# Kernel tuning notes

Measured on AMD Instinct MI355X. Metric: run time of the kernel, lower is better.

Reference implementation:

```python
import jax, jax.numpy as jnp
import numpy as np

NUM_CONN = 8

def _ein_reduce(f):
    # Einstein t-norm fold over last axis: T(a,b) = ab / (2 - (a+b-ab))
    acc = f[..., 0]
    for i in range(1, f.shape[-1]):
        b = f[..., i]
        ab = acc * b
        acc = ab / (2.0 - (acc + b - ab))
    return acc

def _coein_reduce(f):
    # Einstein t-conorm fold over last axis: S(a,b) = (a+b) / (1 + ab)
    acc = f[..., 0]
    for i in range(1, f.shape[-1]):
        b = f[..., i]
        acc = (acc + b) / (1.0 + acc * b)
    return acc

def _ddlg_layer(x, w, idx, is_train):
    # x: [B, in], idx: [out, C] int, w: [out, 4]
    feats = x[:, idx]                      # [B, out, C] gather
    ops = jnp.stack([
        jnp.min(feats, axis=-1),
        jnp.max(feats, axis=-1),
        _ein_reduce(feats),
        _coein_reduce(feats),
    ], axis=-1)                            # [B, out, 4]
    if is_train:
        prob = jax.nn.softmax(w, axis=-1)  # [out, 4]
    else:
        prob = jax.nn.one_hot(jnp.argmax(w, axis=-1), 4, dtype=x.dtype)
    return jnp.einsum('bof,of->bo', ops, prob)

def setup_inputs() -> dict:
    key = jax.random.key(0)
    ks = jax.random.split(key, 6)
    sizes = [4096, 2048, 1024, 2048, 4096]
    x = jax.random.uniform(ks[0], (4096, sizes[0]), dtype=jnp.float32)
    ws = [jax.random.normal(ks[1 + i], (sizes[i + 1], 4), dtype=jnp.float32) for i in range(4)]
    rng = np.random.default_rng(0)
    idxs = []
    for i in range(4):
        # randperm-without-replacement per output neuron
        perm = np.argsort(rng.random((sizes[i + 1], sizes[i])), axis=-1)[:, :NUM_CONN]
        idxs.append(jnp.asarray(perm, dtype=jnp.int32))
    return {
        'x': x,
        'w0': ws[0], 'w1': ws[1], 'w2': ws[2], 'w3': ws[3],
        'idx0': idxs[0], 'idx1': idxs[1], 'idx2': idxs[2], 'idx3': idxs[3],
        'is_train': 1,
    }

def reference(x, w0, w1, w2, w3, idx0, idx1, idx2, idx3, is_train):
    h = _ddlg_layer(x, w0, idx0, is_train)
    h = _ddlg_layer(h, w1, idx1, is_train)
    h = _ddlg_layer(h, w2, idx2, is_train)
    h = _ddlg_layer(h, w3, idx3, is_train)
    return h
```

## Files before the change

kernel.cpp:

```cpp
#include <hip/hip_runtime.h>


typedef _Float16 h2 __attribute__((ext_vector_type(2)));
typedef _Float16 h4 __attribute__((ext_vector_type(4)));

__device__ __forceinline__ float fastrcp(float x) { return __builtin_amdgcn_rcpf(x); }
__device__ __forceinline__ _Float16 hrcp(_Float16 x) {
#if __has_builtin(__builtin_amdgcn_rcph)
    return __builtin_amdgcn_rcph(x);
#else
    return (_Float16)__builtin_amdgcn_rcpf((float)x);
#endif
}
__device__ __forceinline__ unsigned packh2(float a, float b) {
    h2 v = {(_Float16)a, (_Float16)b};
    return __builtin_bit_cast(unsigned, v);
}
__device__ __forceinline__ h2 ash2(unsigned u) { return __builtin_bit_cast(h2, u); }

__device__ __forceinline__ unsigned pk_min(unsigned a, unsigned b) {
    unsigned d; asm("v_pk_min_f16 %0, %1, %2" : "=v"(d) : "v"(a), "v"(b)); return d;
}
__device__ __forceinline__ unsigned pk_max(unsigned a, unsigned b) {
    unsigned d; asm("v_pk_max_f16 %0, %1, %2" : "=v"(d) : "v"(a), "v"(b)); return d;
}
__device__ __forceinline__ unsigned pk_mul(unsigned a, unsigned b) {
    unsigned d; asm("v_pk_mul_f16 %0, %1, %2" : "=v"(d) : "v"(a), "v"(b)); return d;
}
__device__ __forceinline__ unsigned pk_add(unsigned a, unsigned b) {
    unsigned d; asm("v_pk_add_f16 %0, %1, %2" : "=v"(d) : "v"(a), "v"(b)); return d;
}
__device__ __forceinline__ unsigned pk_sub(unsigned a, unsigned b) {
    unsigned d;
    asm("v_pk_add_f16 %0, %1, %2 neg_lo:[0,1] neg_hi:[0,1]" : "=v"(d) : "v"(a), "v"(b));
    return d;
}
__device__ __forceinline__ unsigned pk_fma(unsigned a, unsigned b, unsigned c) {
    unsigned d;
    asm("v_pk_fma_f16 %0, %1, %2, %3" : "=v"(d) : "v"(a), "v"(b), "v"(c));
    return d;
}
__device__ __forceinline__ unsigned pk_fnma(unsigned a, unsigned b, unsigned c) {
    unsigned d;
    asm("v_pk_fma_f16 %0, %1, %2, %3 neg_lo:[1,0,0] neg_hi:[1,0,0]"
        : "=v"(d) : "v"(a), "v"(b), "v"(c));
    return d;
}
__device__ __forceinline__ unsigned pk_mul_blo(unsigned a, unsigned b) {
    unsigned d;
    asm("v_pk_mul_f16 %0, %1, %2 op_sel:[0,0] op_sel_hi:[1,0]" : "=v"(d) : "v"(a), "v"(b));
    return d;
}
__device__ __forceinline__ unsigned pk_fma_bhi(unsigned a, unsigned b, unsigned c) {
    unsigned d;
    asm("v_pk_fma_f16 %0, %1, %2, %3 op_sel:[0,1,0] op_sel_hi:[1,1,1]"
        : "=v"(d) : "v"(a), "v"(b), "v"(c));
    return d;
}

#define PK_ONE 0x3C003C00u
#define PK_TWO 0x40004000u

__global__ __launch_bounds__(256) void prep_k(const float* __restrict__ w0,
                                              const float* __restrict__ w1,
                                              const float* __restrict__ w2,
                                              const float* __restrict__ w3,
                                              const int* __restrict__ is_train,
                                              h4* __restrict__ probsH) {
    const int g = blockIdx.x * 256 + threadIdx.x;
    const float* w; int o;
    if (g < 2048)      { w = w0; o = g; }
    else if (g < 3072) { w = w1; o = g - 2048; }
    else if (g < 5120) { w = w2; o = g - 3072; }
    else               { w = w3; o = g - 5120; }
    float wv[4];
#pragma unroll
    for (int c = 0; c < 4; ++c) wv[c] = w[(o << 2) + c];
    float p[4];
    if (*is_train) {
        float m = fmaxf(fmaxf(wv[0], wv[1]), fmaxf(wv[2], wv[3]));
        float s = 0.0f;
#pragma unroll
        for (int c = 0; c < 4; ++c) { p[c] = __expf(wv[c] - m); s += p[c]; }
        float inv = fastrcp(s);
#pragma unroll
        for (int c = 0; c < 4; ++c) p[c] *= inv;
    } else {
        int a = 0; float best = wv[0];
#pragma unroll
        for (int c = 1; c < 4; ++c) if (wv[c] > best) { best = wv[c]; a = c; }
#pragma unroll
        for (int c = 0; c < 4; ++c) p[c] = (c == a) ? 1.0f : 0.0f;
    }
    probsH[g] = h4{(_Float16)p[0], (_Float16)p[1], (_Float16)p[2], (_Float16)p[3]};
}

struct Chain { unsigned mn0, mn1, mx0, mx1, De0, De1, Ne0, Ne1, Nc0, Nc1, Dc0, Dc1; };

__device__ __forceinline__ void cinit(Chain& C, uint2 v) {
    C.mn0 = v.x; C.mx0 = v.x; C.De0 = v.x;
    C.Ne0 = pk_sub(PK_TWO, v.x); C.Nc0 = pk_add(PK_ONE, v.x); C.Dc0 = pk_sub(PK_ONE, v.x);
    C.mn1 = v.y; C.mx1 = v.y; C.De1 = v.y;
    C.Ne1 = pk_sub(PK_TWO, v.y); C.Nc1 = pk_add(PK_ONE, v.y); C.Dc1 = pk_sub(PK_ONE, v.y);
}
__device__ __forceinline__ void cstep(Chain& C, uint2 v) {
    C.mn0 = pk_min(C.mn0, v.x);            C.mn1 = pk_min(C.mn1, v.y);
    C.mx0 = pk_max(C.mx0, v.x);            C.mx1 = pk_max(C.mx1, v.y);
    C.De0 = pk_mul(C.De0, v.x);            C.De1 = pk_mul(C.De1, v.y);
    const unsigned w0 = pk_sub(PK_TWO, v.x), w1 = pk_sub(PK_TWO, v.y);
    C.Ne0 = pk_mul(C.Ne0, w0);             C.Ne1 = pk_mul(C.Ne1, w1);
    C.Nc0 = pk_fma(C.Nc0, v.x, C.Nc0);     C.Nc1 = pk_fma(C.Nc1, v.y, C.Nc1);
    C.Dc0 = pk_fnma(C.Dc0, v.x, C.Dc0);    C.Dc1 = pk_fnma(C.Dc1, v.y, C.Dc1);
}

__device__ __forceinline__ unsigned finale_half(unsigned mn, unsigned mx,
                                                unsigned De, unsigned Ne,
                                                unsigned Nc, unsigned Dc,
                                                unsigned P01, unsigned P23) {
    const unsigned s1 = pk_add(Ne, De);
    const unsigned s2 = pk_add(Nc, Dc);
    const unsigned d1 = pk_sub(Nc, Dc);
    const unsigned ss = pk_mul(s1, s2);
    const h2 ssh = ash2(ss);
    h2 rh = {hrcp(ssh[0]), hrcp(ssh[1])};
    const unsigned r  = __builtin_bit_cast(unsigned, rh);
    const unsigned t1 = pk_mul(pk_add(De, De), s2);
    const unsigned t2 = pk_mul(d1, s1);
    const unsigned num  = pk_fma_bhi(t2, P23, pk_mul_blo(t1, P23));
    const unsigned base = pk_fma_bhi(mx, P01, pk_mul_blo(mn, P01));
    return pk_fma(num, r, base);
}

__device__ __forceinline__ uint2 finale(const Chain& C, uint2 P) {
    return uint2{finale_half(C.mn0, C.mx0, C.De0, C.Ne0, C.Nc0, C.Dc0, P.x, P.y),
                 finale_half(C.mn1, C.mx1, C.De1, C.Ne1, C.Nc1, C.Dc1, P.x, P.y)};
}

__device__ __forceinline__ uint2 gate(const uint2* __restrict__ rows,
                                      const int4* __restrict__ idx,
                                      const uint2* __restrict__ probs, int o) {
    const int4 i0 = idx[o * 2], i1 = idx[o * 2 + 1];
    const uint2 P = probs[o];
    uint2 A[8];
    A[0] = rows[i0.x]; A[1] = rows[i0.y]; A[2] = rows[i0.z]; A[3] = rows[i0.w];
    A[4] = rows[i1.x]; A[5] = rows[i1.y]; A[6] = rows[i1.z]; A[7] = rows[i1.w];
    Chain C; cinit(C, A[0]);
#pragma unroll
    for (int c = 1; c < 8; ++c) cstep(C, A[c]);
    return finale(C, P);
}

__global__ __launch_bounds__(1024, 8) void ddlg_fused(const float* __restrict__ x,
                                                      const uint2* __restrict__ probsH,
                                                      const int4* __restrict__ idx0,
                                                      const int4* __restrict__ idx1,
                                                      const int4* __restrict__ idx2,
                                                      const int4* __restrict__ idx3,
                                                      float* __restrict__ out) {
    __shared__ __align__(16) _Float16 lds[24576];
    const int t  = threadIdx.x;
    const int b0 = blockIdx.x << 2;

    const uint2* xl  = (const uint2*)lds;
    const uint2* h0v = (const uint2*)(lds + 16384);
    const uint2* h1v = (const uint2*)lds;
    const uint2* h2v = (const uint2*)(lds + 16384);
    uint2* const h0w = (uint2*)(lds + 16384);
    uint2* const h1w = (uint2*)lds;

#pragma unroll
    for (int c = 0; c < 4; ++c) {
        const int j = (c << 10) + t;
        const float v0 = x[(size_t)(b0 + 0) * 4096 + j];
        const float v1 = x[(size_t)(b0 + 1) * 4096 + j];
        const float v2 = x[(size_t)(b0 + 2) * 4096 + j];
        const float v3 = x[(size_t)(b0 + 3) * 4096 + j];
        ((uint2*)lds)[j] = uint2{packh2(v0, v1), packh2(v2, v3)};
    }
    __syncthreads();

#pragma unroll
    for (int k = 0; k < 2; ++k) {
        const int o = (k << 10) + t;
        h0w[o] = gate(xl, idx0, probsH, o);
    }
    __syncthreads();

    h1w[t] = gate(h0v, idx1, probsH + 2048, t);
    __syncthreads();

#pragma unroll
    for (int k = 0; k < 2; ++k) {
        const int o = (k << 10) + t;
        h0w[o] = gate(h1v, idx2, probsH + 3072, o);
    }
    __syncthreads();

#pragma unroll
    for (int k = 0; k < 4; ++k) {
        const int o = (k << 10) + t;
        uint2 r = gate(h2v, idx3, probsH + 5120, o);
        h2 lo = ash2(r.x), hi = ash2(r.y);
        out[(size_t)(b0 + 0) * 4096 + o] = (float)lo[0];
        out[(size_t)(b0 + 1) * 4096 + o] = (float)lo[1];
        out[(size_t)(b0 + 2) * 4096 + o] = (float)hi[0];
        out[(size_t)(b0 + 3) * 4096 + o] = (float)hi[1];
    }
}

extern "C" void kernel_launch(void* const* d_in, const int* in_sizes, int n_in,
                              void* d_out, int out_size, void* d_ws, size_t ws_size,
                              hipStream_t stream) {
    const float* x        = (const float*)d_in[0];
    const float* w0       = (const float*)d_in[1];
    const float* w1       = (const float*)d_in[2];
    const float* w2       = (const float*)d_in[3];
    const float* w3       = (const float*)d_in[4];
    const int4*  idx0     = (const int4*)d_in[5];
    const int4*  idx1     = (const int4*)d_in[6];
    const int4*  idx2     = (const int4*)d_in[7];
    const int4*  idx3     = (const int4*)d_in[8];
    const int*   is_train = (const int*)d_in[9];
    float*       out      = (float*)d_out;

    h4* probsH = (h4*)d_ws;

    prep_k<<<36, 256, 0, stream>>>(w0, w1, w2, w3, is_train, probsH);
    ddlg_fused<<<1024, 1024, 0, stream>>>(x, (const uint2*)probsH,
                                          idx0, idx1, idx2, idx3, out);
}
```

Before: 161.3 us.

## Software-pipeline index/prob loads across gates and vectorize LDS and output stores

Splits the gate into separate index-load, gather, and compute steps. Each gate's global index and probability loads are now issued one step early, overlapping their latency with the previous gate's compute, with compiler fences holding that order. Each thread now handles contiguous output neurons (2t, 2t+1 or 4t..4t+3), so LDS writes become 128-bit and the final global stores become float4. This raises register pressure from holding prefetched index sets, and the per-thread output mapping changes the LDS access pattern of each layer.

```diff
diff --git a/kernel.cpp b/kernel.cpp
--- a/kernel.cpp
+++ b/kernel.cpp
@@ -17,6 +17,8 @@
     return __builtin_bit_cast(unsigned, v);
 }
 __device__ __forceinline__ h2 ash2(unsigned u) { return __builtin_bit_cast(h2, u); }
+
+#define FENCE() asm volatile("" ::: "memory")
 
 __device__ __forceinline__ unsigned pk_min(unsigned a, unsigned b) {
     unsigned d; asm("v_pk_min_f16 %0, %1, %2" : "=v"(d) : "v"(a), "v"(b)); return d;
@@ -131,23 +133,29 @@
     return pk_fma(num, r, base);
 }
 
-__device__ __forceinline__ uint2 finale(const Chain& C, uint2 P) {
+struct IP { int4 i0, i1; uint2 P; };
+
+__device__ __forceinline__ IP load_ip(const int4* __restrict__ idx,
+                                      const uint2* __restrict__ probs, int o) {
+    IP p;
+    p.i0 = idx[o * 2];
+    p.i1 = idx[o * 2 + 1];
+    p.P  = probs[o];
+    return p;
+}
+
+__device__ __forceinline__ void gath(uint2 A[8], const uint2* __restrict__ rows,
+                                     const IP& p) {
+    A[0] = rows[p.i0.x]; A[1] = rows[p.i0.y]; A[2] = rows[p.i0.z]; A[3] = rows[p.i0.w];
+    A[4] = rows[p.i1.x]; A[5] = rows[p.i1.y]; A[6] = rows[p.i1.z]; A[7] = rows[p.i1.w];
+}
+
+__device__ __forceinline__ uint2 run_gate(const uint2 A[8], uint2 P) {
+    Chain C; cinit(C, A[0]);
+#pragma unroll
+    for (int c = 1; c < 8; ++c) cstep(C, A[c]);
     return uint2{finale_half(C.mn0, C.mx0, C.De0, C.Ne0, C.Nc0, C.Dc0, P.x, P.y),
                  finale_half(C.mn1, C.mx1, C.De1, C.Ne1, C.Nc1, C.Dc1, P.x, P.y)};
-}
-
-__device__ __forceinline__ uint2 gate(const uint2* __restrict__ rows,
-                                      const int4* __restrict__ idx,
-                                      const uint2* __restrict__ probs, int o) {
-    const int4 i0 = idx[o * 2], i1 = idx[o * 2 + 1];
-    const uint2 P = probs[o];
-    uint2 A[8];
-    A[0] = rows[i0.x]; A[1] = rows[i0.y]; A[2] = rows[i0.z]; A[3] = rows[i0.w];
-    A[4] = rows[i1.x]; A[5] = rows[i1.y]; A[6] = rows[i1.z]; A[7] = rows[i1.w];
-    Chain C; cinit(C, A[0]);
-#pragma unroll
-    for (int c = 1; c < 8; ++c) cstep(C, A[c]);
-    return finale(C, P);
 }
 
 __global__ __launch_bounds__(1024, 8) void ddlg_fused(const float* __restrict__ x,
@@ -165,8 +173,16 @@
     const uint2* h0v = (const uint2*)(lds + 16384);
     const uint2* h1v = (const uint2*)lds;
     const uint2* h2v = (const uint2*)(lds + 16384);
-    uint2* const h0w = (uint2*)(lds + 16384);
-    uint2* const h1w = (uint2*)lds;
+    uint4* const hw128 = (uint4*)(lds + 16384);
+    uint2* const h1w   = (uint2*)lds;
+
+    const uint2* pr0 = probsH;
+    const uint2* pr1 = probsH + 2048;
+    const uint2* pr2 = probsH + 3072;
+    const uint2* pr3 = probsH + 5120;
+
+    IP qa = load_ip(idx0, pr0, 2 * t);
+    IP qb = load_ip(idx0, pr0, 2 * t + 1);
 
 #pragma unroll
     for (int c = 0; c < 4; ++c) {
@@ -179,32 +195,74 @@
     }
     __syncthreads();
 
-#pragma unroll
-    for (int k = 0; k < 2; ++k) {
-        const int o = (k << 10) + t;
-        h0w[o] = gate(xl, idx0, probsH, o);
-    }
-    __syncthreads();
-
-    h1w[t] = gate(h0v, idx1, probsH + 2048, t);
-    __syncthreads();
-
-#pragma unroll
-    for (int k = 0; k < 2; ++k) {
-        const int o = (k << 10) + t;
-        h0w[o] = gate(h1v, idx2, probsH + 3072, o);
-    }
-    __syncthreads();
-
-#pragma unroll
-    for (int k = 0; k < 4; ++k) {
-        const int o = (k << 10) + t;
-        uint2 r = gate(h2v, idx3, probsH + 5120, o);
-        h2 lo = ash2(r.x), hi = ash2(r.y);
-        out[(size_t)(b0 + 0) * 4096 + o] = (float)lo[0];
-        out[(size_t)(b0 + 1) * 4096 + o] = (float)lo[1];
-        out[(size_t)(b0 + 2) * 4096 + o] = (float)hi[0];
-        out[(size_t)(b0 + 3) * 4096 + o] = (float)hi[1];
+    uint2 A[8];
+
+    {
+        gath(A, xl, qa);
+        IP qc = load_ip(idx1, pr1, t);
+        FENCE();
+        uint2 rA = run_gate(A, qa.P);
+        gath(A, xl, qb);
+        qa = load_ip(idx2, pr2, 2 * t);
+        FENCE();
+        uint2 rB = run_gate(A, qb.P);
+        hw128[t] = uint4{rA.x, rA.y, rB.x, rB.y};
+        qb = qc;
+    }
+    __syncthreads();
+
+    {
+        gath(A, h0v, qb);
+        IP qc = load_ip(idx2, pr2, 2 * t + 1);
+        FENCE();
+        uint2 r = run_gate(A, qb.P);
+        h1w[t] = r;
+        qb = qc;
+    }
+    __syncthreads();
+
+    {
+        gath(A, h1v, qa);
+        IP qc = load_ip(idx3, pr3, 4 * t);
+        FENCE();
+        uint2 rA = run_gate(A, qa.P);
+        gath(A, h1v, qb);
+        qa = load_ip(idx3, pr3, 4 * t + 1);
+        FENCE();
+        uint2 rB = run_gate(A, qb.P);
+        hw128[t] = uint4{rA.x, rA.y, rB.x, rB.y};
+        qb = qc;
+    }
+    __syncthreads();
+
+    {
+        gath(A, h2v, qb);
+        IP qc = load_ip(idx3, pr3, 4 * t + 2);
+        FENCE();
+        uint2 r0 = run_gate(A, qb.P);
+        gath(A, h2v, qa);
+        IP qd = load_ip(idx3, pr3, 4 * t + 3);
+        FENCE();
+        uint2 r1 = run_gate(A, qa.P);
+        gath(A, h2v, qc);
+        FENCE();
+        uint2 r2 = run_gate(A, qc.P);
+        gath(A, h2v, qd);
+        uint2 r3 = run_gate(A, qd.P);
+
+        h2 l0 = ash2(r0.x), h0_ = ash2(r0.y);
+        h2 l1 = ash2(r1.x), h1_ = ash2(r1.y);
+        h2 l2 = ash2(r2.x), h2_ = ash2(r2.y);
+        h2 l3 = ash2(r3.x), h3_ = ash2(r3.y);
+        const int j0 = t << 2;
+        *(float4*)(out + (size_t)(b0 + 0) * 4096 + j0) =
+            make_float4((float)l0[0], (float)l1[0], (float)l2[0], (float)l3[0]);
+        *(float4*)(out + (size_t)(b0 + 1) * 4096 + j0) =
+            make_float4((float)l0[1], (float)l1[1], (float)l2[1], (float)l3[1]);
+        *(float4*)(out + (size_t)(b0 + 2) * 4096 + j0) =
+            make_float4((float)h0_[0], (float)h1_[0], (float)h2_[0], (float)h3_[0]);
+        *(float4*)(out + (size_t)(b0 + 3) * 4096 + j0) =
+            make_float4((float)h0_[1], (float)h1_[1], (float)h2_[1], (float)h3_[1]);
     }
 }
 
```

After: 169.6 us. 5.1% more time.
